# Kernel optimization log

Measured on AMD Instinct MI355X. Metric: run time of the kernel, lower is better.

The kernel has to match this reference:

```python
import jax, jax.numpy as jnp
import numpy as np

N = 131072   # flattened batch*positions
K = 1024     # num_embeddings
D = 128      # embedding_dim
COMMITMENT_COST = 0.25


def setup_inputs() -> dict:
    key = jax.random.key(0)
    k1, k2 = jax.random.split(key)
    inputs = jax.random.normal(k1, (N, D), dtype=jnp.float32)
    # torch init: uniform(-1/num_embeddings, 1/num_embeddings)
    codebook = jax.random.uniform(k2, (K, D), dtype=jnp.float32,
                                  minval=-1.0 / K, maxval=1.0 / K)
    return {"inputs": inputs, "codebook": codebook}


def reference(inputs, codebook):
    distances = (jnp.sum(inputs ** 2, axis=1, keepdims=True)
                 + jnp.sum(codebook ** 2, axis=1)
                 - 2.0 * inputs @ codebook.T)
    encoding_indices = jnp.argmin(distances, axis=1)          # [N]
    quantized = codebook[encoding_indices]                    # [N, D] gather

    q_loss = jnp.mean((quantized - jax.lax.stop_gradient(inputs)) ** 2)
    e_loss = jnp.mean((jax.lax.stop_gradient(quantized) - inputs) ** 2)
    vq_loss = q_loss + COMMITMENT_COST * e_loss

    # straight-through estimator
    quantized_st = inputs + jax.lax.stop_gradient(quantized - inputs)
    return quantized_st, vq_loss, encoding_indices[:, None]
```

## Files before the change

kernel.cpp:

```cpp
#include <hip/hip_runtime.h>

#define N_ROWS 131072
#define K_CODES 1024
#define D_DIM 128
#define MARGIN 5.0e-5f
#define CAND_MARGIN 4.0e-5f

typedef __attribute__((ext_vector_type(8)))  short short8;
typedef __attribute__((ext_vector_type(4)))  float f32x4;


__device__ __forceinline__ unsigned short bf16_rn(float f) {
    unsigned u = __float_as_uint(f);
    unsigned r = u + 0x7fffu + ((u >> 16) & 1u);
    return (unsigned short)(r >> 16);
}
__device__ __forceinline__ float bf16_to_f(unsigned short h) {
    return __uint_as_float(((unsigned)h) << 16);
}

__device__ __forceinline__ float np_sumsq_128(const float* __restrict__ p) {
    float r[8];
    #pragma unroll
    for (int j = 0; j < 8; ++j) r[j] = __fmul_rn(p[j], p[j]);
    #pragma unroll
    for (int i = 8; i < 128; i += 8)
        #pragma unroll
        for (int j = 0; j < 8; ++j)
            r[j] = __fadd_rn(r[j], __fmul_rn(p[i + j], p[i + j]));
    float t01 = __fadd_rn(r[0], r[1]), t23 = __fadd_rn(r[2], r[3]);
    float t45 = __fadd_rn(r[4], r[5]), t67 = __fadd_rn(r[6], r[7]);
    return __fadd_rn(__fadd_rn(t01, t23), __fadd_rn(t45, t67));
}

__device__ __forceinline__ float score_f32(const float* __restrict__ e,
                                           const float* __restrict__ xr, float nn) {
    float a0 = 0.f, a1 = 0.f, a2 = 0.f, a3 = 0.f;
    #pragma unroll
    for (int d = 0; d < D_DIM; d += 4) {
        f32x4 ev = *(const f32x4*)(e + d);
        a0 = fmaf(xr[d + 0], ev.x, a0);
        a1 = fmaf(xr[d + 1], ev.y, a1);
        a2 = fmaf(xr[d + 2], ev.z, a2);
        a3 = fmaf(xr[d + 3], ev.w, a3);
    }
    return fmaf(-2.f, (a0 + a1) + (a2 + a3), nn);
}

__device__ __forceinline__ float quant_score(const float* __restrict__ e,
                                             const float* __restrict__ xr,
                                             float A, float nn) {
    double dotd = 0.0;
    #pragma unroll
    for (int d = 0; d < D_DIM; ++d)
        dotd = fma((double)e[d], (double)xr[d], dotd);
    float M  = (float)dotd;
    float t1 = __fadd_rn(A, nn);
    return __fsub_rn(t1, 2.0f * M);
}

__global__ void vq_n2(const float* __restrict__ cb, float* __restrict__ n2) {
    int code = blockIdx.x * 256 + threadIdx.x;
    n2[code] = np_sumsq_128(cb + (size_t)code * D_DIM);
}

__global__ void vq_split(const float* __restrict__ cb, unsigned short* __restrict__ EH,
                         unsigned short* __restrict__ EL) {
    int i = blockIdx.x * 256 + threadIdx.x;
    float e = cb[i];
    unsigned short h = bf16_rn(e);
    float fl = e - bf16_to_f(h);
    EH[i] = h;
    EL[i] = bf16_rn(fl);
}

__launch_bounds__(256, 2)
__global__ void vq_mfma(const float* __restrict__ x,
                        const unsigned short* __restrict__ EH,
                        const unsigned short* __restrict__ EL,
                        const float* __restrict__ n2,
                        unsigned* __restrict__ best_idx,
                        unsigned* __restrict__ work_list,
                        unsigned* __restrict__ work_count) {
    const int lane = threadIdx.x & 63;
    const int wid  = threadIdx.x >> 6;
    const int q    = lane >> 4;
    const int col  = lane & 15;
    const int rbase = blockIdx.x * 256 + wid * 64;

    short8 xh[4][4], xl[4][4];
    #pragma unroll
    for (int r = 0; r < 4; ++r) {
        const float* xrow = x + (size_t)(rbase + 16 * r + col) * D_DIM;
        #pragma unroll
        for (int k = 0; k < 4; ++k) {
            const float* p = xrow + k * 32 + q * 8;
            f32x4 v0 = *(const f32x4*)p;
            f32x4 v1 = *(const f32x4*)(p + 4);
            float f[8] = {v0.x, v0.y, v0.z, v0.w, v1.x, v1.y, v1.z, v1.w};
            short8 h, l;
            #pragma unroll
            for (int j = 0; j < 8; ++j) {
                unsigned short hb = bf16_rn(f[j]);
                float fl = f[j] - bf16_to_f(hb);
                h[j] = (short)hb;
                l[j] = (short)bf16_rn(fl);
            }
            xh[r][k] = h; xl[r][k] = l;
        }
    }

    float b1[4], b2[4], b3[4];
    unsigned i1[4], i2[4];
    #pragma unroll
    for (int r = 0; r < 4; ++r) {
        b1[r] = b2[r] = b3[r] = 3.0e38f;
        i1[r] = i2[r] = 0;
    }

    for (int ct = 0; ct < K_CODES / 16; ++ct) {
        const unsigned short* ph = EH + ((size_t)(ct * 16 + col)) * D_DIM + q * 8;
        const unsigned short* pl = EL + ((size_t)(ct * 16 + col)) * D_DIM + q * 8;

        f32x4 acc[4];
        #pragma unroll
        for (int r = 0; r < 4; ++r) acc[r] = (f32x4){0.f, 0.f, 0.f, 0.f};

        #pragma unroll
        for (int k = 0; k < 4; ++k) {
            short8 eh = *(const short8*)(ph + k * 32);
            short8 el = *(const short8*)(pl + k * 32);
            #pragma unroll
            for (int r = 0; r < 4; ++r) {
                acc[r] = __builtin_amdgcn_mfma_f32_16x16x32_bf16(eh, xh[r][k], acc[r], 0, 0, 0);
                acc[r] = __builtin_amdgcn_mfma_f32_16x16x32_bf16(eh, xl[r][k], acc[r], 0, 0, 0);
                acc[r] = __builtin_amdgcn_mfma_f32_16x16x32_bf16(el, xh[r][k], acc[r], 0, 0, 0);
            }
        }

        f32x4 nn = *(const f32x4*)(n2 + ct * 16 + q * 4);
        #pragma unroll
        for (int r = 0; r < 4; ++r) {
            #pragma unroll
            for (int g = 0; g < 4; ++g) {
                float v = fmaf(-2.0f, acc[r][g], nn[g]);
                unsigned c = (unsigned)(ct * 16 + q * 4 + g);
                bool lt1 = v < b1[r];
                bool lt2 = v < b2[r];
                bool lt3 = v < b3[r];
                b3[r] = lt2 ? b2[r] : (lt3 ? v : b3[r]);
                b2[r] = lt1 ? b1[r] : (lt2 ? v : b2[r]);
                i2[r] = lt1 ? i1[r] : (lt2 ? c : i2[r]);
                b1[r] = lt1 ? v : b1[r];
                i1[r] = lt1 ? c : i1[r];
            }
        }
    }

    #pragma unroll
    for (int r = 0; r < 4; ++r) {
        #pragma unroll
        for (int m = 16; m <= 32; m <<= 1) {
            float    oa1 = __shfl_xor(b1[r], m), oa2 = __shfl_xor(b2[r], m), oa3 = __shfl_xor(b3[r], m);
            unsigned oj1 = __shfl_xor(i1[r], m), oj2 = __shfl_xor(i2[r], m);
            bool t1 = (oa1 < b1[r]) || (oa1 == b1[r] && oj1 < i1[r]);
            float    m1 = t1 ? oa1 : b1[r];
            unsigned w1 = t1 ? oj1 : i1[r];
            float    ha = t1 ? b1[r] : b2[r];   unsigned iha = t1 ? i1[r] : i2[r];
            float    hb = t1 ? oa2   : oa1;     unsigned ihb = t1 ? oj2   : oj1;
            bool t2 = (hb < ha) || (hb == ha && ihb < iha);
            float    m2 = t2 ? hb : ha;
            unsigned w2 = t2 ? ihb : iha;
            float ha2 = t2 ? ha : (t1 ? b2[r] : b3[r]);
            float hb2 = t2 ? (t1 ? oa3 : oa2) : hb;
            float m3 = fminf(ha2, hb2);
            b1[r] = m1; i1[r] = w1; b2[r] = m2; i2[r] = w2; b3[r] = m3;
        }
        if (lane < 16) {
            int row = rbase + 16 * r + lane;
            best_idx[row] = i1[r];
            if (b2[r] - b1[r] < MARGIN) {
                bool full = (b3[r] - b1[r] < MARGIN);
                unsigned p = atomicAdd(work_count, 1u);
                work_list[p] = (unsigned)row | (i2[r] << 17) | (full ? 0x80000000u : 0u);
            }
        }
    }
}

__launch_bounds__(256, 1)
__global__ void vq_pair(const float* __restrict__ x, const float* __restrict__ cb,
                        const float* __restrict__ n2,
                        const unsigned* __restrict__ work_count,
                        const unsigned* __restrict__ work_list,
                        unsigned* __restrict__ best_idx) {
    const unsigned gid = blockIdx.x * 256 + threadIdx.x;
    const unsigned n = *work_count;
    for (unsigned p = gid; p < n; p += 65536) {
        unsigned e = work_list[p];
        if (e & 0x80000000u) continue;
        unsigned row = e & 0x1FFFFu;
        unsigned c2  = (e >> 17) & 0x3FFu;
        unsigned c1  = best_idx[row];

        float xr[D_DIM];
        #pragma unroll
        for (int i = 0; i < D_DIM / 4; ++i) {
            f32x4 v = ((const f32x4*)(x + (size_t)row * D_DIM))[i];
            xr[4 * i + 0] = v.x; xr[4 * i + 1] = v.y;
            xr[4 * i + 2] = v.z; xr[4 * i + 3] = v.w;
        }
        float A = np_sumsq_128(xr);
        float dq1 = quant_score(cb + (size_t)c1 * D_DIM, xr, A, n2[c1]);
        float dq2 = quant_score(cb + (size_t)c2 * D_DIM, xr, A, n2[c2]);
        unsigned win = (dq2 < dq1 || (dq2 == dq1 && c2 < c1)) ? c2 : c1;
        best_idx[row] = win;
    }
}

__launch_bounds__(256, 1)
__global__ void vq_full(const float* __restrict__ x, const float* __restrict__ cb,
                        const float* __restrict__ n2,
                        const unsigned* __restrict__ work_count,
                        const unsigned* __restrict__ work_list,
                        unsigned* __restrict__ best_idx) {
    const int lane = threadIdx.x & 63;
    const unsigned gw = blockIdx.x * 4 + (threadIdx.x >> 6);
    const unsigned n = *work_count;
    for (unsigned wi = gw; wi < n; wi += 1024) {
        unsigned e = work_list[wi];
        if (!(e & 0x80000000u)) continue;
        unsigned row = e & 0x1FFFFu;
        const float* xrow = x + (size_t)row * D_DIM;

        float xr[D_DIM];
        #pragma unroll
        for (int i = 0; i < D_DIM / 4; ++i) {
            f32x4 v = ((const f32x4*)xrow)[i];
            xr[4 * i + 0] = v.x; xr[4 * i + 1] = v.y;
            xr[4 * i + 2] = v.z; xr[4 * i + 3] = v.w;
        }
        float A = np_sumsq_128(xr);

        float smin = 3.0e38f;
        #pragma unroll 1
        for (int j = 0; j < K_CODES / 64; ++j) {
            unsigned c = (unsigned)lane * (K_CODES / 64) + j;
            smin = fminf(smin, score_f32(cb + (size_t)c * D_DIM, xr, n2[c]));
        }
        float b1w = smin;
        #pragma unroll
        for (int m = 1; m < 64; m <<= 1) b1w = fminf(b1w, __shfl_xor(b1w, m));

        float bestq = 3.0e38f; unsigned bi = 0xffffffffu;
        #pragma unroll 1
        for (int j = 0; j < K_CODES / 64; ++j) {
            unsigned c = (unsigned)lane * (K_CODES / 64) + j;
            float s = score_f32(cb + (size_t)c * D_DIM, xr, n2[c]);
            if (s < b1w + CAND_MARGIN) {
                float dq = quant_score(cb + (size_t)c * D_DIM, xr, A, n2[c]);
                if (dq < bestq) { bestq = dq; bi = c; }
            }
        }
        #pragma unroll
        for (int m = 1; m < 64; m <<= 1) {
            float    ob = __shfl_xor(bestq, m);
            unsigned oi = __shfl_xor(bi, m);
            if (ob < bestq || (ob == bestq && oi < bi)) { bestq = ob; bi = oi; }
        }
        if (lane == 0) best_idx[row] = bi;
    }
}

__global__ void vq_out(const float* __restrict__ x, const float* __restrict__ cb,
                       const unsigned* __restrict__ best_idx, float* __restrict__ out,
                       double* __restrict__ partials) {
    const int t = threadIdx.x;
    const int rloc = t >> 5;
    const int q = t & 31;
    double lsum = 0.0;
    for (int it = 0; it < N_ROWS / (1024 * 8); ++it) {
        int row = it * (1024 * 8) + blockIdx.x * 8 + rloc;
        unsigned idx = best_idx[row];
        float4 xv = ((const float4*)x)[(size_t)row * 32 + q];
        float4 ev = ((const float4*)cb)[(size_t)idx * 32 + q];
        float dx = ev.x - xv.x, dy = ev.y - xv.y, dz = ev.z - xv.z, dw = ev.w - xv.w;
        float4 o;
        o.x = xv.x + dx; o.y = xv.y + dy; o.z = xv.z + dz; o.w = xv.w + dw;
        ((float4*)out)[(size_t)row * 32 + q] = o;
        lsum += (double)dx * dx + (double)dy * dy + (double)dz * dz + (double)dw * dw;
        if (q == 0) out[(size_t)N_ROWS * D_DIM + 1 + row] = (float)idx;
    }
    #pragma unroll
    for (int m = 32; m >= 1; m >>= 1) lsum += __shfl_xor(lsum, m);
    __shared__ double wsum[4];
    if ((t & 63) == 0) wsum[t >> 6] = lsum;
    __syncthreads();
    if (t == 0) partials[blockIdx.x] = wsum[0] + wsum[1] + wsum[2] + wsum[3];
}

__global__ void vq_fin(const double* __restrict__ partials, float* __restrict__ out) {
    int t = threadIdx.x;
    double s = partials[t] + partials[t + 256] + partials[t + 512] + partials[t + 768];
    #pragma unroll
    for (int m = 32; m >= 1; m >>= 1) s += __shfl_xor(s, m);
    __shared__ double wsum[4];
    if ((t & 63) == 0) wsum[t >> 6] = s;
    __syncthreads();
    if (t == 0) {
        double total = wsum[0] + wsum[1] + wsum[2] + wsum[3];
        out[(size_t)N_ROWS * D_DIM] = (float)(1.25 * total / ((double)N_ROWS * D_DIM));
    }
}

extern "C" void kernel_launch(void* const* d_in, const int* in_sizes, int n_in,
                              void* d_out, int out_size, void* d_ws, size_t ws_size,
                              hipStream_t stream) {
    const float* x  = (const float*)d_in[0];
    const float* cb = (const float*)d_in[1];
    float* out = (float*)d_out;
    char* ws = (char*)d_ws;

    unsigned*       work_count = (unsigned*)ws;
    float*          n2         = (float*)(ws + 1024);
    unsigned*       best_idx   = (unsigned*)(ws + 8192);
    unsigned*       work_list  = (unsigned*)(ws + 8192 + 524288);
    double*         partials   = (double*)(ws + 8192 + 2 * 524288);
    unsigned short* EH         = (unsigned short*)(ws + 1064960);
    unsigned short* EL         = (unsigned short*)(ws + 1327104);

    hipMemsetAsync(ws, 0, 1024, stream);
    vq_n2    <<<K_CODES / 256, 256, 0, stream>>>(cb, n2);
    vq_split <<<K_CODES * D_DIM / 256, 256, 0, stream>>>(cb, EH, EL);
    vq_mfma  <<<N_ROWS / 256, 256, 0, stream>>>(x, EH, EL, n2, best_idx, work_list, work_count);
    vq_pair  <<<256, 256, 0, stream>>>(x, cb, n2, work_count, work_list, best_idx);
    vq_full  <<<256, 256, 0, stream>>>(x, cb, n2, work_count, work_list, best_idx);
    vq_out   <<<1024, 256, 0, stream>>>(x, cb, best_idx, out, partials);
    vq_fin   <<<1, 256, 0, stream>>>(partials, out);
}
```

Measured before the change: 362.2 us.

## Halve rows per wave, fold -2 and norms into MFMA, merge fixup kernels

Each wave now handles 32 rows instead of 64, cutting register use so launch bounds can rise to 4 blocks per CU, with twice as many blocks launched. The -2 scale moves into the bf16 codebook split and the accumulators start from the code norms, which removes the per-score fma. The top-3 tracking uses med3/min, and the lane offset is added to the indices once after the loop. The pair and full fixup kernels become one resolve kernel, and the memset is replaced by zeroing the counter inside vq_n2, saving launches. The trade-off is that each codebook load is reused across fewer rows, and near-tie behaviour may shift slightly because the bf16 rounding of the scaled codebook differs.

```diff
diff --git a/kernel.cpp b/kernel.cpp
--- a/kernel.cpp
+++ b/kernel.cpp
@@ -59,7 +59,9 @@
     return __fsub_rn(t1, 2.0f * M);
 }
 
-__global__ void vq_n2(const float* __restrict__ cb, float* __restrict__ n2) {
+__global__ void vq_n2(const float* __restrict__ cb, float* __restrict__ n2,
+                      unsigned* __restrict__ work_count) {
+    if (blockIdx.x == 0 && threadIdx.x == 0) *work_count = 0;
     int code = blockIdx.x * 256 + threadIdx.x;
     n2[code] = np_sumsq_128(cb + (size_t)code * D_DIM);
 }
@@ -67,14 +69,14 @@
 __global__ void vq_split(const float* __restrict__ cb, unsigned short* __restrict__ EH,
                          unsigned short* __restrict__ EL) {
     int i = blockIdx.x * 256 + threadIdx.x;
-    float e = cb[i];
+    float e = -2.0f * cb[i];
     unsigned short h = bf16_rn(e);
     float fl = e - bf16_to_f(h);
     EH[i] = h;
     EL[i] = bf16_rn(fl);
 }
 
-__launch_bounds__(256, 2)
+__launch_bounds__(256, 4)
 __global__ void vq_mfma(const float* __restrict__ x,
                         const unsigned short* __restrict__ EH,
                         const unsigned short* __restrict__ EL,
@@ -86,11 +88,11 @@
     const int wid  = threadIdx.x >> 6;
     const int q    = lane >> 4;
     const int col  = lane & 15;
-    const int rbase = blockIdx.x * 256 + wid * 64;
-
-    short8 xh[4][4], xl[4][4];
-    #pragma unroll
-    for (int r = 0; r < 4; ++r) {
+    const int rbase = blockIdx.x * 128 + wid * 32;
+
+    short8 xh[2][4], xl[2][4];
+    #pragma unroll
+    for (int r = 0; r < 2; ++r) {
         const float* xrow = x + (size_t)(rbase + 16 * r + col) * D_DIM;
         #pragma unroll
         for (int k = 0; k < 4; ++k) {
@@ -110,10 +112,10 @@
         }
     }
 
-    float b1[4], b2[4], b3[4];
-    unsigned i1[4], i2[4];
-    #pragma unroll
-    for (int r = 0; r < 4; ++r) {
+    float b1[2], b2[2], b3[2];
+    unsigned i1[2], i2[2];
+    #pragma unroll
+    for (int r = 0; r < 2; ++r) {
         b1[r] = b2[r] = b3[r] = 3.0e38f;
         i1[r] = i2[r] = 0;
     }
@@ -122,43 +124,44 @@
         const unsigned short* ph = EH + ((size_t)(ct * 16 + col)) * D_DIM + q * 8;
         const unsigned short* pl = EL + ((size_t)(ct * 16 + col)) * D_DIM + q * 8;
 
-        f32x4 acc[4];
-        #pragma unroll
-        for (int r = 0; r < 4; ++r) acc[r] = (f32x4){0.f, 0.f, 0.f, 0.f};
+        f32x4 nn = *(const f32x4*)(n2 + ct * 16 + q * 4);
+        f32x4 acc[2];
+        acc[0] = nn; acc[1] = nn;
 
         #pragma unroll
         for (int k = 0; k < 4; ++k) {
             short8 eh = *(const short8*)(ph + k * 32);
             short8 el = *(const short8*)(pl + k * 32);
             #pragma unroll
-            for (int r = 0; r < 4; ++r) {
+            for (int r = 0; r < 2; ++r) {
                 acc[r] = __builtin_amdgcn_mfma_f32_16x16x32_bf16(eh, xh[r][k], acc[r], 0, 0, 0);
                 acc[r] = __builtin_amdgcn_mfma_f32_16x16x32_bf16(eh, xl[r][k], acc[r], 0, 0, 0);
                 acc[r] = __builtin_amdgcn_mfma_f32_16x16x32_bf16(el, xh[r][k], acc[r], 0, 0, 0);
             }
         }
 
-        f32x4 nn = *(const f32x4*)(n2 + ct * 16 + q * 4);
-        #pragma unroll
-        for (int r = 0; r < 4; ++r) {
+        #pragma unroll
+        for (int r = 0; r < 2; ++r) {
             #pragma unroll
             for (int g = 0; g < 4; ++g) {
-                float v = fmaf(-2.0f, acc[r][g], nn[g]);
-                unsigned c = (unsigned)(ct * 16 + q * 4 + g);
-                bool lt1 = v < b1[r];
-                bool lt2 = v < b2[r];
-                bool lt3 = v < b3[r];
-                b3[r] = lt2 ? b2[r] : (lt3 ? v : b3[r]);
-                b2[r] = lt1 ? b1[r] : (lt2 ? v : b2[r]);
-                i2[r] = lt1 ? i1[r] : (lt2 ? c : i2[r]);
-                b1[r] = lt1 ? v : b1[r];
-                i1[r] = lt1 ? c : i1[r];
-            }
-        }
-    }
-
-    #pragma unroll
-    for (int r = 0; r < 4; ++r) {
+                float s = acc[r][g];
+                unsigned cl = (unsigned)(ct * 16 + g);
+                bool lt1 = s < b1[r];
+                bool lt2 = s < b2[r];
+                float nb3 = __builtin_amdgcn_fmed3f(b2[r], b3[r], s);
+                float nb2 = __builtin_amdgcn_fmed3f(b1[r], b2[r], s);
+                float nb1 = fminf(b1[r], s);
+                i2[r] = lt1 ? i1[r] : (lt2 ? cl : i2[r]);
+                i1[r] = lt1 ? cl : i1[r];
+                b3[r] = nb3; b2[r] = nb2; b1[r] = nb1;
+            }
+        }
+    }
+
+    #pragma unroll
+    for (int r = 0; r < 2; ++r) {
+        i1[r] += (unsigned)(q * 4);
+        i2[r] += (unsigned)(q * 4);
         #pragma unroll
         for (int m = 16; m <= 32; m <<= 1) {
             float    oa1 = __shfl_xor(b1[r], m), oa2 = __shfl_xor(b2[r], m), oa3 = __shfl_xor(b3[r], m);
@@ -189,48 +192,17 @@
 }
 
 __launch_bounds__(256, 1)
-__global__ void vq_pair(const float* __restrict__ x, const float* __restrict__ cb,
-                        const float* __restrict__ n2,
-                        const unsigned* __restrict__ work_count,
-                        const unsigned* __restrict__ work_list,
-                        unsigned* __restrict__ best_idx) {
-    const unsigned gid = blockIdx.x * 256 + threadIdx.x;
-    const unsigned n = *work_count;
-    for (unsigned p = gid; p < n; p += 65536) {
-        unsigned e = work_list[p];
-        if (e & 0x80000000u) continue;
-        unsigned row = e & 0x1FFFFu;
-        unsigned c2  = (e >> 17) & 0x3FFu;
-        unsigned c1  = best_idx[row];
-
-        float xr[D_DIM];
-        #pragma unroll
-        for (int i = 0; i < D_DIM / 4; ++i) {
-            f32x4 v = ((const f32x4*)(x + (size_t)row * D_DIM))[i];
-            xr[4 * i + 0] = v.x; xr[4 * i + 1] = v.y;
-            xr[4 * i + 2] = v.z; xr[4 * i + 3] = v.w;
-        }
-        float A = np_sumsq_128(xr);
-        float dq1 = quant_score(cb + (size_t)c1 * D_DIM, xr, A, n2[c1]);
-        float dq2 = quant_score(cb + (size_t)c2 * D_DIM, xr, A, n2[c2]);
-        unsigned win = (dq2 < dq1 || (dq2 == dq1 && c2 < c1)) ? c2 : c1;
-        best_idx[row] = win;
-    }
-}
-
-__launch_bounds__(256, 1)
-__global__ void vq_full(const float* __restrict__ x, const float* __restrict__ cb,
-                        const float* __restrict__ n2,
-                        const unsigned* __restrict__ work_count,
-                        const unsigned* __restrict__ work_list,
-                        unsigned* __restrict__ best_idx) {
+__global__ void vq_resolve(const float* __restrict__ x, const float* __restrict__ cb,
+                           const float* __restrict__ n2,
+                           const unsigned* __restrict__ work_count,
+                           const unsigned* __restrict__ work_list,
+                           unsigned* __restrict__ best_idx) {
     const int lane = threadIdx.x & 63;
     const unsigned gw = blockIdx.x * 4 + (threadIdx.x >> 6);
     const unsigned n = *work_count;
-    for (unsigned wi = gw; wi < n; wi += 1024) {
-        unsigned e = work_list[wi];
-        if (!(e & 0x80000000u)) continue;
-        unsigned row = e & 0x1FFFFu;
+    for (unsigned wi = gw; wi < n; wi += 2048) {
+        const unsigned e = work_list[wi];
+        const unsigned row = e & 0x1FFFFu;
         const float* xrow = x + (size_t)row * D_DIM;
 
         float xr[D_DIM];
@@ -242,33 +214,42 @@
         }
         float A = np_sumsq_128(xr);
 
-        float smin = 3.0e38f;
-        #pragma unroll 1
-        for (int j = 0; j < K_CODES / 64; ++j) {
-            unsigned c = (unsigned)lane * (K_CODES / 64) + j;
-            smin = fminf(smin, score_f32(cb + (size_t)c * D_DIM, xr, n2[c]));
-        }
-        float b1w = smin;
-        #pragma unroll
-        for (int m = 1; m < 64; m <<= 1) b1w = fminf(b1w, __shfl_xor(b1w, m));
-
-        float bestq = 3.0e38f; unsigned bi = 0xffffffffu;
-        #pragma unroll 1
-        for (int j = 0; j < K_CODES / 64; ++j) {
-            unsigned c = (unsigned)lane * (K_CODES / 64) + j;
-            float s = score_f32(cb + (size_t)c * D_DIM, xr, n2[c]);
-            if (s < b1w + CAND_MARGIN) {
-                float dq = quant_score(cb + (size_t)c * D_DIM, xr, A, n2[c]);
-                if (dq < bestq) { bestq = dq; bi = c; }
-            }
-        }
-        #pragma unroll
-        for (int m = 1; m < 64; m <<= 1) {
-            float    ob = __shfl_xor(bestq, m);
-            unsigned oi = __shfl_xor(bi, m);
-            if (ob < bestq || (ob == bestq && oi < bi)) { bestq = ob; bi = oi; }
-        }
-        if (lane == 0) best_idx[row] = bi;
+        if (!(e & 0x80000000u)) {
+            unsigned c2 = (e >> 17) & 0x3FFu;
+            unsigned c1 = best_idx[row];
+            float dq1 = quant_score(cb + (size_t)c1 * D_DIM, xr, A, n2[c1]);
+            float dq2 = quant_score(cb + (size_t)c2 * D_DIM, xr, A, n2[c2]);
+            unsigned win = (dq2 < dq1 || (dq2 == dq1 && c2 < c1)) ? c2 : c1;
+            if (lane == 0) best_idx[row] = win;
+        } else {
+            float smin = 3.0e38f;
+            #pragma unroll 1
+            for (int j = 0; j < K_CODES / 64; ++j) {
+                unsigned c = (unsigned)lane * (K_CODES / 64) + j;
+                smin = fminf(smin, score_f32(cb + (size_t)c * D_DIM, xr, n2[c]));
+            }
+            float b1w = smin;
+            #pragma unroll
+            for (int m = 1; m < 64; m <<= 1) b1w = fminf(b1w, __shfl_xor(b1w, m));
+
+            float bestq = 3.0e38f; unsigned bi = 0xffffffffu;
+            #pragma unroll 1
+            for (int j = 0; j < K_CODES / 64; ++j) {
+                unsigned c = (unsigned)lane * (K_CODES / 64) + j;
+                float s = score_f32(cb + (size_t)c * D_DIM, xr, n2[c]);
+                if (s < b1w + CAND_MARGIN) {
+                    float dq = quant_score(cb + (size_t)c * D_DIM, xr, A, n2[c]);
+                    if (dq < bestq) { bestq = dq; bi = c; }
+                }
+            }
+            #pragma unroll
+            for (int m = 1; m < 64; m <<= 1) {
+                float    ob = __shfl_xor(bestq, m);
+                unsigned oi = __shfl_xor(bi, m);
+                if (ob < bestq || (ob == bestq && oi < bi)) { bestq = ob; bi = oi; }
+            }
+            if (lane == 0) best_idx[row] = bi;
+        }
     }
 }
 
@@ -329,12 +310,10 @@
     unsigned short* EH         = (unsigned short*)(ws + 1064960);
     unsigned short* EL         = (unsigned short*)(ws + 1327104);
 
-    hipMemsetAsync(ws, 0, 1024, stream);
-    vq_n2    <<<K_CODES / 256, 256, 0, stream>>>(cb, n2);
-    vq_split <<<K_CODES * D_DIM / 256, 256, 0, stream>>>(cb, EH, EL);
-    vq_mfma  <<<N_ROWS / 256, 256, 0, stream>>>(x, EH, EL, n2, best_idx, work_list, work_count);
-    vq_pair  <<<256, 256, 0, stream>>>(x, cb, n2, work_count, work_list, best_idx);
-    vq_full  <<<256, 256, 0, stream>>>(x, cb, n2, work_count, work_list, best_idx);
-    vq_out   <<<1024, 256, 0, stream>>>(x, cb, best_idx, out, partials);
-    vq_fin   <<<1, 256, 0, stream>>>(partials, out);
-}
+    vq_n2     <<<K_CODES / 256, 256, 0, stream>>>(cb, n2, work_count);
+    vq_split  <<<K_CODES * D_DIM / 256, 256, 0, stream>>>(cb, EH, EL);
+    vq_mfma   <<<N_ROWS / 128, 256, 0, stream>>>(x, EH, EL, n2, best_idx, work_list, work_count);
+    vq_resolve<<<512, 256, 0, stream>>>(x, cb, n2, work_count, work_list, best_idx);
+    vq_out    <<<1024, 256, 0, stream>>>(x, cb, best_idx, out, partials);
+    vq_fin    <<<1, 256, 0, stream>>>(partials, out);
+}
```

Result: slower. 449.8 us (+24.2%).
